# Performance work log

Measured on AMD Instinct MI355X. Metric: run time of the kernel, lower is better.

The kernel has to match this reference:

```python
import jax, jax.numpy as jnp
import numpy as np

B, L, T = 8, 1024, 10
K = 1.0                 # soft_sign sharpness (config.k)
S = float(np.log(9.0))  # self.s
W_PEN = 1.0             # self.w


def soft_sign(x):
    return jax.nn.sigmoid(2.0 * K * x)


def mlp2(f, W1, b1, W2, b2):
    # pointwise 2-layer MLP with ReLU after each layer; output dim 1 -> squeeze
    h = jax.nn.relu(jnp.einsum('...i,oi->...o', f, W1) + b1)
    return jax.nn.relu(jnp.einsum('...i,oi->...o', h, W2) + b2)[..., 0]


def setup_inputs() -> dict:
    key = jax.random.key(0)
    ks = jax.random.split(key, 16)
    u = jax.random.normal(ks[0], (B, L, L), jnp.float32)
    x = jax.random.uniform(ks[1], (B, L, 4), jnp.float32)
    p = lambda k, s: (jax.random.normal(k, s, jnp.float32) * 0.5)
    return dict(
        u=u, x=x, timesteps=T,
        aW1=p(ks[2], (T, 3, 3)), ab1=p(ks[3], (T, 3)), aW2=p(ks[4], (T, 1, 3)), ab2=p(ks[5], (T, 1)),
        rW1=p(ks[6], (T, 3, 3)), rb1=p(ks[7], (T, 3)), rW2=p(ks[8], (T, 1, 3)), rb2=p(ks[9], (T, 1)),
        lW1=p(ks[10], (T, 3, 2)), lb1=p(ks[11], (T, 3)), lW2=p(ks[12], (T, 1, 3)), lb2=p(ks[13], (T, 1)),
    )


def reference(u, x, timesteps, aW1, ab1, aW2, ab2, rW1, rb1, rW2, rb2, lW1, lb1, lW2, lb2):
    # constraint matrix m: sum of symmetrized outer products of base channels
    ba, bu, bc, bg = x[:, :, 0], x[:, :, 1], x[:, :, 2], x[:, :, 3]
    def sym_outer(p, q):
        o = jnp.einsum('bi,bj->bij', p, q)
        return o + o.swapaxes(-1, -2)
    m = sym_outer(ba, bu) + sym_outer(bc, bg) + sym_outer(bu, bg)

    def contact(ah):
        aa = ah * ah
        return (aa + aa.swapaxes(-1, -2)) * 0.5 * m

    uu = soft_sign(u - S) * u
    a_hat = jax.nn.sigmoid(uu) * soft_sign(uu - S)
    a = contact(a_hat)
    lmbd = W_PEN * jax.nn.relu(jnp.sum(a, -1) - 1.0)

    outs = []
    for t in range(timesteps):  # fixed unroll, distinct params per step
        grad_a = -uu * 0.5 + (lmbd * soft_sign(jnp.sum(a, -1) - 1.0))[..., None]
        grad = a_hat * m * (grad_a + grad_a.swapaxes(-1, -2))
        feats = jnp.stack([a_hat, grad, uu], -1)  # [B,L,L,3]
        ah_new = mlp2(feats, aW1[t], ab1[t], aW2[t], ab2[t])
        rho = mlp2(feats, rW1[t], rb1[t], rW2[t], rb2[t])
        ah_new = jnp.clip(jax.nn.relu(jnp.abs(ah_new) - rho), -1.0, 1.0)
        a = contact(ah_new)
        lg = jax.nn.relu(jnp.sum(a, -1) - 1.0)
        lmbd = mlp2(jnp.stack([lmbd, lg], -1), lW1[t], lb1[t], lW2[t], lb2[t])
        a_hat = ah_new
        outs.append(a)
    return jnp.stack(outs)  # [T,B,L,L] == a_t_list[1:]
```

## Files before the change

### kernel.cpp

```cpp
#include <hip/hip_runtime.h>
#include <hip/hip_bf16.h>

#define BB 8
#define LL 1024
#define TT 10
#define TILE 64
#define NTILE 16
#define NOFF 120
#define NBLK 1024
#define S_CONST 2.1972245773362196f

typedef __hip_bfloat16 bf16;

static __device__ __forceinline__ float sigm(float v) {
    return 1.0f / (1.0f + __expf(-v));
}
static __device__ __forceinline__ unsigned short f2bf(float v) {
    bf16 h = __float2bfloat16(v);
    unsigned short b; __builtin_memcpy(&b, &h, 2); return b;
}
static __device__ __forceinline__ float lo2f(unsigned int v) { return __uint_as_float(v << 16); }
static __device__ __forceinline__ float hi2f(unsigned int v) { return __uint_as_float(v & 0xffff0000u); }
static __device__ __forceinline__ unsigned int pk2(float uu, float ah) {
    return (unsigned int)f2bf(uu) | ((unsigned int)f2bf(ah) << 16);
}

#define RAWBAR() do { asm volatile("s_waitcnt lgkmcnt(0)" ::: "memory"); \
                      __builtin_amdgcn_s_barrier(); } while (0)

static __device__ __forceinline__ void wait_done(const unsigned int* dcnt) {
    for (int it = 0; it < (1 << 20); ++it) {
        if (__hip_atomic_load(dcnt, __ATOMIC_RELAXED, __HIP_MEMORY_SCOPE_AGENT) >= 16u)
            break;
        __builtin_amdgcn_s_sleep(4);
    }
}

static __device__ __forceinline__ float mlp3(float f0, float f1, float f2, const float* w) {
    float h0 = fmaxf(w[0]*f0 + w[1]*f1 + w[2]*f2 + w[9],  0.0f);
    float h1 = fmaxf(w[3]*f0 + w[4]*f1 + w[5]*f2 + w[10], 0.0f);
    float h2 = fmaxf(w[6]*f0 + w[7]*f1 + w[8]*f2 + w[11], 0.0f);
    return fmaxf(w[12]*h0 + w[13]*h1 + w[14]*h2 + w[15], 0.0f);
}
static __device__ __forceinline__ float ahnew_calc(float ah, float grad, float uuv, const float* w) {
    float va = mlp3(ah, grad, uuv, w);
    float vr = mlp3(ah, grad, uuv, w + 16);
    float v = fmaxf(fabsf(va) - vr, 0.0f);
    return fminf(v, 1.0f);
}

#define LOAD_W(tt) do { if (tid < 32) { int _t = (tt); float v; \
    if      (tid <  9) v = aW1[_t*9 + tid]; \
    else if (tid < 12) v = ab1[_t*3 + (tid-9)]; \
    else if (tid < 15) v = aW2[_t*3 + (tid-12)]; \
    else if (tid < 16) v = ab2[_t]; \
    else if (tid < 25) v = rW1[_t*9 + (tid-16)]; \
    else if (tid < 28) v = rb1[_t*3 + (tid-25)]; \
    else if (tid < 31) v = rW2[_t*3 + (tid-28)]; \
    else               v = rb2[_t]; \
    w[tid] = v; } } while (0)

#define LAMBDA_PHASE(ROWI, ROWJ) do { if (tid < 128) { \
    int row = (tid < 64) ? ((ROWI) + tid) : ((ROWJ) + tid - 64); \
    float rsv = __hip_atomic_load(&rs_cur[b*LL + row], __ATOMIC_RELAXED, __HIP_MEMORY_SCOPE_AGENT); \
    float lg = fmaxf(rsv - 1.0f, 0.0f); \
    if (t == 0) lam = lg; \
    else { int o = t - 1; \
        float h0 = fmaxf(lW1[o*6+0]*lam + lW1[o*6+1]*lg + lb1[o*3+0], 0.0f); \
        float h1 = fmaxf(lW1[o*6+2]*lam + lW1[o*6+3]*lg + lb1[o*3+1], 0.0f); \
        float h2 = fmaxf(lW1[o*6+4]*lam + lW1[o*6+5]*lg + lb1[o*3+2], 0.0f); \
        lam = fmaxf(lW2[o*3+0]*h0 + lW2[o*3+1]*h1 + lW2[o*3+2]*h2 + lb2[o], 0.0f); } \
    float lsv = lam * sigm(2.0f*(rsv - 1.0f)); \
    if (tid < 64) { lsI[tid] = lsv; rsIb[tid] = 0.0f; } \
    else          { lsJ[tid-64] = lsv; rsJb[tid-64] = 0.0f; } } } while (0)

__global__ __launch_bounds__(256, 4) void k_main(
        const float* __restrict__ u, const float* __restrict__ x,
        float* __restrict__ rs, unsigned int* __restrict__ done,
        float* __restrict__ out,
        const float* __restrict__ aW1, const float* __restrict__ ab1,
        const float* __restrict__ aW2, const float* __restrict__ ab2,
        const float* __restrict__ rW1, const float* __restrict__ rb1,
        const float* __restrict__ rW2, const float* __restrict__ rb2,
        const float* __restrict__ lW1, const float* __restrict__ lb1,
        const float* __restrict__ lW2, const float* __restrict__ lb2) {
    __shared__ unsigned int stA[TILE * 65];
    __shared__ unsigned int stB[TILE * 65];
    __shared__ float buf[16 * 65];
    __shared__ float xIl[4 * TILE];
    __shared__ float lsI[TILE], lsJ[TILE];
    __shared__ float rsIb[TILE], rsJb[TILE];
    __shared__ float w[32];

    int gid = blockIdx.x, tid = threadIdx.x;
    int c = tid & 63, rg = tid >> 6;
    float lam = 0.0f;

    if (gid < BB * NOFF) {
        int b = gid / NOFF, po = gid % NOFF;
        int i = 0; while (po >= NTILE - 1 - i) { po -= NTILE - 1 - i; i++; }
        int I = i, J = i + 1 + po;
        int Ib = I * TILE, Jb = J * TILE;

        float xc0 = x[((size_t)b*LL + Jb + c)*4 + 0], xc1 = x[((size_t)b*LL + Jb + c)*4 + 1];
        float xc2 = x[((size_t)b*LL + Jb + c)*4 + 2], xc3 = x[((size_t)b*LL + Jb + c)*4 + 3];
        float bu_c = xc1, bg_c = xc3, s1_c = xc0 + xc3, s2_c = xc2 + xc1;
        { int row = tid >> 2, k2 = tid & 3;
          xIl[k2*TILE + row] = x[((size_t)b*LL + Ib + row)*4 + k2]; }

        size_t ubIJ = ((size_t)b*LL + Ib)*LL + Jb;
        size_t ubJI = ((size_t)b*LL + Jb)*LL + Ib;
        #pragma unroll
        for (int k = 0; k < 16; k++) {
            int r = rg + 4*k;
            float uv  = u[ubIJ + (size_t)r*LL + c];
            float uuv = sigm(2.0f*(uv - S_CONST))*uv;
            float ah  = sigm(uuv)*sigm(2.0f*(uuv - S_CONST));
            stA[r*65 + c] = pk2(uuv, ah);
            uv  = u[ubJI + (size_t)r*LL + c];
            uuv = sigm(2.0f*(uv - S_CONST))*uv;
            ah  = sigm(uuv)*sigm(2.0f*(uuv - S_CONST));
            stB[r*65 + c] = pk2(uuv, ah);
        }
        if (tid < 64) rsIb[tid] = 0.0f; else if (tid < 128) rsJb[tid-64] = 0.0f;
        __syncthreads();

        {
            float aval[16]; float rsJacc = 0.0f;
            #pragma unroll
            for (int k = 0; k < 16; k++) {
                int r = rg + 4*k;
                float ah_ij = hi2f(stA[r*65 + c]);
                float ah_ji = hi2f(stB[c*65 + r]);
                float m = xIl[0*TILE+r]*bu_c + xIl[2*TILE+r]*bg_c
                        + xIl[1*TILE+r]*s1_c + xIl[3*TILE+r]*s2_c;
                float a0 = 0.5f*(ah_ij*ah_ij + ah_ji*ah_ji)*m;
                aval[k] = a0; rsJacc += a0;
            }
            atomicAdd(&rsJb[c], rsJacc);
            #pragma unroll
            for (int p = 0; p < 4; p++) {
                #pragma unroll
                for (int kk = 0; kk < 4; kk++) { int jj = rg + 4*kk; buf[jj*65 + c] = aval[4*p + kk]; }
                RAWBAR();
                { int jj = tid & 15, cc0 = tid >> 4;
                  float part = 0.0f;
                  #pragma unroll
                  for (int s = 0; s < 4; s++) part += buf[jj*65 + (cc0 + 16*s)];
                  atomicAdd(&rsIb[16*p + jj], part); }
                RAWBAR();
            }
            if (tid < 64) atomicAdd(&rs[b*LL + Ib + tid], rsIb[tid]);
            else if (tid < 128) atomicAdd(&rs[b*LL + Jb + (tid-64)], rsJb[tid-64]);
            if (tid < 128) {
                asm volatile("s_waitcnt vmcnt(0)" ::: "memory");
                if (tid == 0)
                    __hip_atomic_fetch_add(&done[(0*128 + b*16 + I)*16], 1u, __ATOMIC_RELAXED, __HIP_MEMORY_SCOPE_AGENT);
                if (tid == 64)
                    __hip_atomic_fetch_add(&done[(0*128 + b*16 + J)*16], 1u, __ATOMIC_RELAXED, __HIP_MEMORY_SCOPE_AGENT);
            }
        }

        for (int t = 0; t < TT; t++) {
            LOAD_W(t);
            if (tid == 0)  wait_done(&done[((size_t)t*128 + b*16 + I)*16]);
            if (tid == 64) wait_done(&done[((size_t)t*128 + b*16 + J)*16]);
            RAWBAR();
            asm volatile("" ::: "memory");
            const float* rs_cur = rs + (size_t)t*BB*LL;
            LAMBDA_PHASE(Ib, Jb);
            RAWBAR();

            size_t outBase = (((size_t)t*BB + b)*LL)*LL;
            bool last = (t == TT-1);
            float aval[16]; float rsJacc = 0.0f;
            #pragma unroll
            for (int k = 0; k < 16; k++) {
                int r = rg + 4*k;
                unsigned int vA = stA[r*65 + c], vB = stB[c*65 + r];
                float uu_ij = lo2f(vA), ah_ij = hi2f(vA);
                float uu_ji = lo2f(vB), ah_ji = hi2f(vB);
                float m = xIl[0*TILE+r]*bu_c + xIl[2*TILE+r]*bg_c
                        + xIl[1*TILE+r]*s1_c + xIl[3*TILE+r]*s2_c;
                float gsum = -0.5f*(uu_ij + uu_ji) + lsI[r] + lsJ[c];
                float an_ij = ahnew_calc(ah_ij, ah_ij*m*gsum, uu_ij, w);
                float an_ji = ahnew_calc(ah_ji, ah_ji*m*gsum, uu_ji, w);
                float a_val = 0.5f*(an_ij*an_ij + an_ji*an_ji)*m;
                ((unsigned short*)stA)[(r*65 + c)*2 + 1] = f2bf(an_ij);
                ((unsigned short*)stB)[(c*65 + r)*2 + 1] = f2bf(an_ji);
                __builtin_nontemporal_store(a_val, &out[outBase + (size_t)(Ib+r)*LL + (Jb+c)]);
                aval[k] = a_val; rsJacc += a_val;
            }
            atomicAdd(&rsJb[c], rsJacc);

            #pragma unroll
            for (int p = 0; p < 4; p++) {
                #pragma unroll
                for (int kk = 0; kk < 4; kk++) { int jj = rg + 4*kk; buf[jj*65 + c] = aval[4*p + kk]; }
                RAWBAR();
                { int jj = tid & 15, cc0 = tid >> 4;
                  float part = 0.0f;
                  #pragma unroll
                  for (int s = 0; s < 4; s++) {
                      int cc = cc0 + 16*s;
                      float v = buf[jj*65 + cc];
                      __builtin_nontemporal_store(v, &out[outBase + (size_t)(Jb+cc)*LL + (Ib + 16*p + jj)]);
                      part += v;
                  }
                  if (!last) atomicAdd(&rsIb[16*p + jj], part); }
                RAWBAR();
            }
            if (!last) {
                float* rs_next = rs + (size_t)(t+1)*BB*LL;
                if (tid < 128) {
                    if (tid < 64) atomicAdd(&rs_next[b*LL + Ib + tid], rsIb[tid]);
                    else          atomicAdd(&rs_next[b*LL + Jb + (tid-64)], rsJb[tid-64]);
                    asm volatile("s_waitcnt vmcnt(0)" ::: "memory");
                    if (tid == 0)
                        __hip_atomic_fetch_add(&done[((size_t)(t+1)*128 + b*16 + I)*16], 1u, __ATOMIC_RELAXED, __HIP_MEMORY_SCOPE_AGENT);
                    if (tid == 64)
                        __hip_atomic_fetch_add(&done[((size_t)(t+1)*128 + b*16 + J)*16], 1u, __ATOMIC_RELAXED, __HIP_MEMORY_SCOPE_AGENT);
                }
            }
        }
    } else {
        int d = gid - BB*NOFF;
        int g0 = 2*d;
        int b = g0 >> 4;
        int TA = g0 & 15, TB = (g0 & 15) + 1;
        int Ab = TA * TILE, Bb = TB * TILE;
        float* xIlB = buf;

        float t0, t1, t2, t3;
        t0 = x[((size_t)b*LL + Ab + c)*4 + 0]; t1 = x[((size_t)b*LL + Ab + c)*4 + 1];
        t2 = x[((size_t)b*LL + Ab + c)*4 + 2]; t3 = x[((size_t)b*LL + Ab + c)*4 + 3];
        float buA = t1, bgA = t3, s1A = t0 + t3, s2A = t2 + t1;
        t0 = x[((size_t)b*LL + Bb + c)*4 + 0]; t1 = x[((size_t)b*LL + Bb + c)*4 + 1];
        t2 = x[((size_t)b*LL + Bb + c)*4 + 2]; t3 = x[((size_t)b*LL + Bb + c)*4 + 3];
        float buB = t1, bgB = t3, s1B = t0 + t3, s2B = t2 + t1;
        { int row = tid >> 2, k2 = tid & 3;
          xIl [k2*TILE + row] = x[((size_t)b*LL + Ab + row)*4 + k2];
          xIlB[k2*TILE + row] = x[((size_t)b*LL + Bb + row)*4 + k2]; }

        size_t ubA = ((size_t)b*LL + Ab)*LL + Ab;
        size_t ubB = ((size_t)b*LL + Bb)*LL + Bb;
        #pragma unroll
        for (int k = 0; k < 16; k++) {
            int r = rg + 4*k;
            float uv  = u[ubA + (size_t)r*LL + c];
            float uuv = sigm(2.0f*(uv - S_CONST))*uv;
            float ah  = sigm(uuv)*sigm(2.0f*(uuv - S_CONST));
            stA[r*65 + c] = pk2(uuv, ah);
            uv  = u[ubB + (size_t)r*LL + c];
            uuv = sigm(2.0f*(uv - S_CONST))*uv;
            ah  = sigm(uuv)*sigm(2.0f*(uuv - S_CONST));
            stB[r*65 + c] = pk2(uuv, ah);
        }
        if (tid < 64) rsIb[tid] = 0.0f; else if (tid < 128) rsJb[tid-64] = 0.0f;
        __syncthreads();
        {
            float accA = 0.0f, accB = 0.0f;
            #pragma unroll
            for (int k = 0; k < 16; k++) {
                int r = rg + 4*k;
                float aij = hi2f(stA[r*65 + c]), aji = hi2f(stA[c*65 + r]);
                float m = xIl[0*TILE+r]*buA + xIl[2*TILE+r]*bgA
                        + xIl[1*TILE+r]*s1A + xIl[3*TILE+r]*s2A;
                accA += 0.5f*(aij*aij + aji*aji)*m;
                aij = hi2f(stB[r*65 + c]); aji = hi2f(stB[c*65 + r]);
                m = xIlB[0*TILE+r]*buB + xIlB[2*TILE+r]*bgB
                  + xIlB[1*TILE+r]*s1B + xIlB[3*TILE+r]*s2B;
                accB += 0.5f*(aij*aij + aji*aji)*m;
            }
            atomicAdd(&rsIb[c], accA);
            atomicAdd(&rsJb[c], accB);
            RAWBAR();
            if (tid < 64) atomicAdd(&rs[b*LL + Ab + tid], rsIb[tid]);
            else if (tid < 128) atomicAdd(&rs[b*LL + Bb + (tid-64)], rsJb[tid-64]);
            if (tid < 128) {
                asm volatile("s_waitcnt vmcnt(0)" ::: "memory");
                if (tid == 0)
                    __hip_atomic_fetch_add(&done[(0*128 + b*16 + TA)*16], 1u, __ATOMIC_RELAXED, __HIP_MEMORY_SCOPE_AGENT);
                if (tid == 64)
                    __hip_atomic_fetch_add(&done[(0*128 + b*16 + TB)*16], 1u, __ATOMIC_RELAXED, __HIP_MEMORY_SCOPE_AGENT);
            }
        }

        for (int t = 0; t < TT; t++) {
            LOAD_W(t);
            if (tid == 0)  wait_done(&done[((size_t)t*128 + b*16 + TA)*16]);
            if (tid == 64) wait_done(&done[((size_t)t*128 + b*16 + TB)*16]);
            RAWBAR();
            asm volatile("" ::: "memory");
            const float* rs_cur = rs + (size_t)t*BB*LL;
            LAMBDA_PHASE(Ab, Bb);
            RAWBAR();

            size_t outBase = (((size_t)t*BB + b)*LL)*LL;
            bool last = (t == TT-1);

            unsigned int vT[16];
            #pragma unroll
            for (int k = 0; k < 16; k++) vT[k] = stA[c*65 + (rg + 4*k)];
            RAWBAR();
            float acc = 0.0f;
            #pragma unroll
            for (int k = 0; k < 16; k++) {
                int r = rg + 4*k;
                unsigned int vO = stA[r*65 + c];
                float uu_ij = lo2f(vO), ah_ij = hi2f(vO);
                float uu_ji = lo2f(vT[k]), ah_ji = hi2f(vT[k]);
                float m = xIl[0*TILE+r]*buA + xIl[2*TILE+r]*bgA
                        + xIl[1*TILE+r]*s1A + xIl[3*TILE+r]*s2A;
                float gsum = -0.5f*(uu_ij + uu_ji) + lsI[r] + lsI[c];
                float an_ij = ahnew_calc(ah_ij, ah_ij*m*gsum, uu_ij, w);
                float an_ji = ahnew_calc(ah_ji, ah_ji*m*gsum, uu_ji, w);
                float a_val = 0.5f*(an_ij*an_ij + an_ji*an_ji)*m;
                ((unsigned short*)stA)[(r*65 + c)*2 + 1] = f2bf(an_ij);
                __builtin_nontemporal_store(a_val, &out[outBase + (size_t)(Ab+r)*LL + (Ab+c)]);
                acc += a_val;
            }
            if (!last) atomicAdd(&rsIb[c], acc);

            #pragma unroll
            for (int k = 0; k < 16; k++) vT[k] = stB[c*65 + (rg + 4*k)];
            RAWBAR();
            acc = 0.0f;
            #pragma unroll
            for (int k = 0; k < 16; k++) {
                int r = rg + 4*k;
                unsigned int vO = stB[r*65 + c];
                float uu_ij = lo2f(vO), ah_ij = hi2f(vO);
                float uu_ji = lo2f(vT[k]), ah_ji = hi2f(vT[k]);
                float m = xIlB[0*TILE+r]*buB + xIlB[2*TILE+r]*bgB
                        + xIlB[1*TILE+r]*s1B + xIlB[3*TILE+r]*s2B;
                float gsum = -0.5f*(uu_ij + uu_ji) + lsJ[r] + lsJ[c];
                float an_ij = ahnew_calc(ah_ij, ah_ij*m*gsum, uu_ij, w);
                float an_ji = ahnew_calc(ah_ji, ah_ji*m*gsum, uu_ji, w);
                float a_val = 0.5f*(an_ij*an_ij + an_ji*an_ji)*m;
                ((unsigned short*)stB)[(r*65 + c)*2 + 1] = f2bf(an_ij);
                __builtin_nontemporal_store(a_val, &out[outBase + (size_t)(Bb+r)*LL + (Bb+c)]);
                acc += a_val;
            }
            if (!last) {
                atomicAdd(&rsJb[c], acc);
                RAWBAR();
                float* rs_next = rs + (size_t)(t+1)*BB*LL;
                if (tid < 128) {
                    if (tid < 64) atomicAdd(&rs_next[b*LL + Ab + tid], rsIb[tid]);
                    else          atomicAdd(&rs_next[b*LL + Bb + (tid-64)], rsJb[tid-64]);
                    asm volatile("s_waitcnt vmcnt(0)" ::: "memory");
                    if (tid == 0)
                        __hip_atomic_fetch_add(&done[((size_t)(t+1)*128 + b*16 + TA)*16], 1u, __ATOMIC_RELAXED, __HIP_MEMORY_SCOPE_AGENT);
                    if (tid == 64)
                        __hip_atomic_fetch_add(&done[((size_t)(t+1)*128 + b*16 + TB)*16], 1u, __ATOMIC_RELAXED, __HIP_MEMORY_SCOPE_AGENT);
                }
            }
        }
    }
}

extern "C" void kernel_launch(void* const* d_in, const int* in_sizes, int n_in,
                              void* d_out, int out_size, void* d_ws, size_t ws_size,
                              hipStream_t stream) {
    const float* u   = (const float*)d_in[0];
    const float* x   = (const float*)d_in[1];
    const float* aW1 = (const float*)d_in[3];
    const float* ab1 = (const float*)d_in[4];
    const float* aW2 = (const float*)d_in[5];
    const float* ab2 = (const float*)d_in[6];
    const float* rW1 = (const float*)d_in[7];
    const float* rb1 = (const float*)d_in[8];
    const float* rW2 = (const float*)d_in[9];
    const float* rb2 = (const float*)d_in[10];
    const float* lW1 = (const float*)d_in[11];
    const float* lb1 = (const float*)d_in[12];
    const float* lW2 = (const float*)d_in[13];
    const float* lb2 = (const float*)d_in[14];
    float* out = (float*)d_out;

    float* rs = (float*)d_ws;
    unsigned int* done = (unsigned int*)(rs + (size_t)TT*BB*LL);
    size_t zbytes = (size_t)TT*BB*LL*sizeof(float) + (size_t)TT*128*16*sizeof(unsigned int);
    hipMemsetAsync(rs, 0, zbytes, stream);

    hipLaunchKernelGGL(k_main, dim3(NBLK), dim3(256), 0, stream,
                       u, x, rs, done, out,
                       aW1, ab1, aW2, ab2, rW1, rb1, rW2, rb2,
                       lW1, lb1, lW2, lb2);
}
```

Before: 551.3 us.

## Keep tile state in registers, one diagonal tile per block, shrink LDS

The per-tile packed (uu, a_hat) state moves out of shared memory into per-thread registers; both the tile and its transpose are held by each thread. Shared memory drops to a single staging buffer, which allows launch bounds of 5 blocks per CU. The row-sum reduction and transposed output store are collapsed from four barrier-separated passes into one. Diagonal work is split into one block per tile instead of pairs, adding 64 blocks. The cost is higher register pressure, which may cause spills under the tighter launch bound.

```diff
diff --git a/kernel.cpp b/kernel.cpp
--- a/kernel.cpp
+++ b/kernel.cpp
@@ -7,7 +7,8 @@
 #define TILE 64
 #define NTILE 16
 #define NOFF 120
-#define NBLK 1024
+#define NOFFT (BB*NOFF)
+#define NBLK (NOFFT + BB*NTILE)
 #define S_CONST 2.1972245773362196f
 
 typedef __hip_bfloat16 bf16;
@@ -34,6 +35,10 @@
             break;
         __builtin_amdgcn_s_sleep(4);
     }
+}
+static __device__ __forceinline__ void add_done(unsigned int* done, int t, int b, int tile) {
+    __hip_atomic_fetch_add(&done[((size_t)t*128 + b*16 + tile)*16], 1u,
+                           __ATOMIC_RELAXED, __HIP_MEMORY_SCOPE_AGENT);
 }
 
 static __device__ __forceinline__ float mlp3(float f0, float f1, float f2, const float* w) {
@@ -60,21 +65,17 @@
     else               v = rb2[_t]; \
     w[tid] = v; } } while (0)
 
-#define LAMBDA_PHASE(ROWI, ROWJ) do { if (tid < 128) { \
-    int row = (tid < 64) ? ((ROWI) + tid) : ((ROWJ) + tid - 64); \
-    float rsv = __hip_atomic_load(&rs_cur[b*LL + row], __ATOMIC_RELAXED, __HIP_MEMORY_SCOPE_AGENT); \
-    float lg = fmaxf(rsv - 1.0f, 0.0f); \
+#define LAM_UPDATE(rsv) do { \
+    float lg = fmaxf((rsv) - 1.0f, 0.0f); \
     if (t == 0) lam = lg; \
     else { int o = t - 1; \
         float h0 = fmaxf(lW1[o*6+0]*lam + lW1[o*6+1]*lg + lb1[o*3+0], 0.0f); \
         float h1 = fmaxf(lW1[o*6+2]*lam + lW1[o*6+3]*lg + lb1[o*3+1], 0.0f); \
         float h2 = fmaxf(lW1[o*6+4]*lam + lW1[o*6+5]*lg + lb1[o*3+2], 0.0f); \
         lam = fmaxf(lW2[o*3+0]*h0 + lW2[o*3+1]*h1 + lW2[o*3+2]*h2 + lb2[o], 0.0f); } \
-    float lsv = lam * sigm(2.0f*(rsv - 1.0f)); \
-    if (tid < 64) { lsI[tid] = lsv; rsIb[tid] = 0.0f; } \
-    else          { lsJ[tid-64] = lsv; rsJb[tid-64] = 0.0f; } } } while (0)
-
-__global__ __launch_bounds__(256, 4) void k_main(
+    } while (0)
+
+__global__ __launch_bounds__(256, 5) void k_main(
         const float* __restrict__ u, const float* __restrict__ x,
         float* __restrict__ rs, unsigned int* __restrict__ done,
         float* __restrict__ out,
@@ -84,30 +85,29 @@
         const float* __restrict__ rW2, const float* __restrict__ rb2,
         const float* __restrict__ lW1, const float* __restrict__ lb1,
         const float* __restrict__ lW2, const float* __restrict__ lb2) {
-    __shared__ unsigned int stA[TILE * 65];
-    __shared__ unsigned int stB[TILE * 65];
-    __shared__ float buf[16 * 65];
+    __shared__ unsigned int bufU[TILE * 65];
     __shared__ float xIl[4 * TILE];
     __shared__ float lsI[TILE], lsJ[TILE];
     __shared__ float rsIb[TILE], rsJb[TILE];
     __shared__ float w[32];
+    float* buff = (float*)bufU;
 
     int gid = blockIdx.x, tid = threadIdx.x;
     int c = tid & 63, rg = tid >> 6;
     float lam = 0.0f;
 
-    if (gid < BB * NOFF) {
+    if (gid < NOFFT) {
         int b = gid / NOFF, po = gid % NOFF;
         int i = 0; while (po >= NTILE - 1 - i) { po -= NTILE - 1 - i; i++; }
         int I = i, J = i + 1 + po;
         int Ib = I * TILE, Jb = J * TILE;
 
-        float xc0 = x[((size_t)b*LL + Jb + c)*4 + 0], xc1 = x[((size_t)b*LL + Jb + c)*4 + 1];
-        float xc2 = x[((size_t)b*LL + Jb + c)*4 + 2], xc3 = x[((size_t)b*LL + Jb + c)*4 + 3];
-        float bu_c = xc1, bg_c = xc3, s1_c = xc0 + xc3, s2_c = xc2 + xc1;
+        float4 xc4 = ((const float4*)x)[(size_t)b*LL + Jb + c];
+        float bu_c = xc4.y, bg_c = xc4.w, s1_c = xc4.x + xc4.w, s2_c = xc4.z + xc4.y;
         { int row = tid >> 2, k2 = tid & 3;
           xIl[k2*TILE + row] = x[((size_t)b*LL + Ib + row)*4 + k2]; }
 
+        unsigned int vIJ[16], vJI[16];
         size_t ubIJ = ((size_t)b*LL + Ib)*LL + Jb;
         size_t ubJI = ((size_t)b*LL + Jb)*LL + Ib;
         #pragma unroll
@@ -116,48 +116,44 @@
             float uv  = u[ubIJ + (size_t)r*LL + c];
             float uuv = sigm(2.0f*(uv - S_CONST))*uv;
             float ah  = sigm(uuv)*sigm(2.0f*(uuv - S_CONST));
-            stA[r*65 + c] = pk2(uuv, ah);
+            vIJ[k] = pk2(uuv, ah);
             uv  = u[ubJI + (size_t)r*LL + c];
             uuv = sigm(2.0f*(uv - S_CONST))*uv;
             ah  = sigm(uuv)*sigm(2.0f*(uuv - S_CONST));
-            stB[r*65 + c] = pk2(uuv, ah);
+            bufU[r*65 + c] = pk2(uuv, ah);
         }
         if (tid < 64) rsIb[tid] = 0.0f; else if (tid < 128) rsJb[tid-64] = 0.0f;
-        __syncthreads();
+        RAWBAR();
+        #pragma unroll
+        for (int k = 0; k < 16; k++) vJI[k] = bufU[c*65 + (rg + 4*k)];
+        RAWBAR();
 
         {
-            float aval[16]; float rsJacc = 0.0f;
+            float rsJacc = 0.0f;
             #pragma unroll
             for (int k = 0; k < 16; k++) {
                 int r = rg + 4*k;
-                float ah_ij = hi2f(stA[r*65 + c]);
-                float ah_ji = hi2f(stB[c*65 + r]);
+                float ah_ij = hi2f(vIJ[k]), ah_ji = hi2f(vJI[k]);
                 float m = xIl[0*TILE+r]*bu_c + xIl[2*TILE+r]*bg_c
                         + xIl[1*TILE+r]*s1_c + xIl[3*TILE+r]*s2_c;
                 float a0 = 0.5f*(ah_ij*ah_ij + ah_ji*ah_ji)*m;
-                aval[k] = a0; rsJacc += a0;
+                buff[r*65 + c] = a0;
+                rsJacc += a0;
             }
             atomicAdd(&rsJb[c], rsJacc);
-            #pragma unroll
-            for (int p = 0; p < 4; p++) {
-                #pragma unroll
-                for (int kk = 0; kk < 4; kk++) { int jj = rg + 4*kk; buf[jj*65 + c] = aval[4*p + kk]; }
-                RAWBAR();
-                { int jj = tid & 15, cc0 = tid >> 4;
-                  float part = 0.0f;
-                  #pragma unroll
-                  for (int s = 0; s < 4; s++) part += buf[jj*65 + (cc0 + 16*s)];
-                  atomicAdd(&rsIb[16*p + jj], part); }
-                RAWBAR();
-            }
+            RAWBAR();
+            { int jj = tid & 63, cc0 = tid >> 6;
+              float part = 0.0f;
+              #pragma unroll
+              for (int s = 0; s < 16; s++) part += buff[jj*65 + (cc0*16 + s)];
+              atomicAdd(&rsIb[jj], part); }
+            RAWBAR();
             if (tid < 64) atomicAdd(&rs[b*LL + Ib + tid], rsIb[tid]);
             else if (tid < 128) atomicAdd(&rs[b*LL + Jb + (tid-64)], rsJb[tid-64]);
             if (tid < 128) {
                 asm volatile("s_waitcnt vmcnt(0)" ::: "memory");
-                if (tid == 0)
-                    __hip_atomic_fetch_add(&done[(0*128 + b*16 + I)*16], 1u, __ATOMIC_RELAXED, __HIP_MEMORY_SCOPE_AGENT);
-                if (tid == 64)
-                    __hip_atomic_fetch_add(&done[(0*128 + b*16 + J)*16], 1u, __ATOMIC_RELAXED, __HIP_MEMORY_SCOPE_AGENT);
+                if (tid == 0)  add_done(done, 0, b, I);
+                if (tid == 64) add_done(done, 0, b, J);
             }
         }
 
@@ -166,18 +162,24 @@
             if (tid == 0)  wait_done(&done[((size_t)t*128 + b*16 + I)*16]);
             if (tid == 64) wait_done(&done[((size_t)t*128 + b*16 + J)*16]);
             RAWBAR();
-            asm volatile("" ::: "memory");
             const float* rs_cur = rs + (size_t)t*BB*LL;
-            LAMBDA_PHASE(Ib, Jb);
+            if (tid < 128) {
+                int row = (tid < 64) ? (Ib + tid) : (Jb + tid - 64);
+                float rsv = __hip_atomic_load(&rs_cur[b*LL + row], __ATOMIC_RELAXED, __HIP_MEMORY_SCOPE_AGENT);
+                LAM_UPDATE(rsv);
+                float lsv = lam * sigm(2.0f*(rsv - 1.0f));
+                if (tid < 64) { lsI[tid] = lsv; rsIb[tid] = 0.0f; }
+                else          { lsJ[tid-64] = lsv; rsJb[tid-64] = 0.0f; }
+            }
             RAWBAR();
 
             size_t outBase = (((size_t)t*BB + b)*LL)*LL;
             bool last = (t == TT-1);
-            float aval[16]; float rsJacc = 0.0f;
+            float rsJacc = 0.0f;
             #pragma unroll
             for (int k = 0; k < 16; k++) {
                 int r = rg + 4*k;
-                unsigned int vA = stA[r*65 + c], vB = stB[c*65 + r];
+                unsigned int vA = vIJ[k], vB = vJI[k];
                 float uu_ij = lo2f(vA), ah_ij = hi2f(vA);
                 float uu_ji = lo2f(vB), ah_ji = hi2f(vB);
                 float m = xIl[0*TILE+r]*bu_c + xIl[2*TILE+r]*bg_c
@@ -186,174 +188,125 @@
                 float an_ij = ahnew_calc(ah_ij, ah_ij*m*gsum, uu_ij, w);
                 float an_ji = ahnew_calc(ah_ji, ah_ji*m*gsum, uu_ji, w);
                 float a_val = 0.5f*(an_ij*an_ij + an_ji*an_ji)*m;
-                ((unsigned short*)stA)[(r*65 + c)*2 + 1] = f2bf(an_ij);
-                ((unsigned short*)stB)[(c*65 + r)*2 + 1] = f2bf(an_ji);
+                vIJ[k] = ((unsigned int)f2bf(an_ij) << 16) | (vA & 0xffffu);
+                vJI[k] = ((unsigned int)f2bf(an_ji) << 16) | (vB & 0xffffu);
                 __builtin_nontemporal_store(a_val, &out[outBase + (size_t)(Ib+r)*LL + (Jb+c)]);
-                aval[k] = a_val; rsJacc += a_val;
-            }
-            atomicAdd(&rsJb[c], rsJacc);
-
-            #pragma unroll
-            for (int p = 0; p < 4; p++) {
-                #pragma unroll
-                for (int kk = 0; kk < 4; kk++) { int jj = rg + 4*kk; buf[jj*65 + c] = aval[4*p + kk]; }
+                buff[r*65 + c] = a_val;
+                rsJacc += a_val;
+            }
+            if (!last) atomicAdd(&rsJb[c], rsJacc);
+            RAWBAR();
+            { int jj = tid & 63, cc0 = tid >> 6;
+              float part = 0.0f;
+              #pragma unroll
+              for (int s = 0; s < 16; s++) {
+                  int cc = cc0*16 + s;
+                  float v = buff[jj*65 + cc];
+                  __builtin_nontemporal_store(v, &out[outBase + (size_t)(Jb+cc)*LL + (Ib + jj)]);
+                  part += v;
+              }
+              if (!last) atomicAdd(&rsIb[jj], part); }
+            if (!last) {
                 RAWBAR();
-                { int jj = tid & 15, cc0 = tid >> 4;
-                  float part = 0.0f;
-                  #pragma unroll
-                  for (int s = 0; s < 4; s++) {
-                      int cc = cc0 + 16*s;
-                      float v = buf[jj*65 + cc];
-                      __builtin_nontemporal_store(v, &out[outBase + (size_t)(Jb+cc)*LL + (Ib + 16*p + jj)]);
-                      part += v;
-                  }
-                  if (!last) atomicAdd(&rsIb[16*p + jj], part); }
-                RAWBAR();
-            }
-            if (!last) {
                 float* rs_next = rs + (size_t)(t+1)*BB*LL;
                 if (tid < 128) {
                     if (tid < 64) atomicAdd(&rs_next[b*LL + Ib + tid], rsIb[tid]);
                     else          atomicAdd(&rs_next[b*LL + Jb + (tid-64)], rsJb[tid-64]);
                     asm volatile("s_waitcnt vmcnt(0)" ::: "memory");
-                    if (tid == 0)
-                        __hip_atomic_fetch_add(&done[((size_t)(t+1)*128 + b*16 + I)*16], 1u, __ATOMIC_RELAXED, __HIP_MEMORY_SCOPE_AGENT);
-                    if (tid == 64)
-                        __hip_atomic_fetch_add(&done[((size_t)(t+1)*128 + b*16 + J)*16], 1u, __ATOMIC_RELAXED, __HIP_MEMORY_SCOPE_AGENT);
+                    if (tid == 0)  add_done(done, t+1, b, I);
+                    if (tid == 64) add_done(done, t+1, b, J);
                 }
             }
         }
     } else {
-        int d = gid - BB*NOFF;
-        int g0 = 2*d;
-        int b = g0 >> 4;
-        int TA = g0 & 15, TB = (g0 & 15) + 1;
-        int Ab = TA * TILE, Bb = TB * TILE;
-        float* xIlB = buf;
-
-        float t0, t1, t2, t3;
-        t0 = x[((size_t)b*LL + Ab + c)*4 + 0]; t1 = x[((size_t)b*LL + Ab + c)*4 + 1];
-        t2 = x[((size_t)b*LL + Ab + c)*4 + 2]; t3 = x[((size_t)b*LL + Ab + c)*4 + 3];
-        float buA = t1, bgA = t3, s1A = t0 + t3, s2A = t2 + t1;
-        t0 = x[((size_t)b*LL + Bb + c)*4 + 0]; t1 = x[((size_t)b*LL + Bb + c)*4 + 1];
-        t2 = x[((size_t)b*LL + Bb + c)*4 + 2]; t3 = x[((size_t)b*LL + Bb + c)*4 + 3];
-        float buB = t1, bgB = t3, s1B = t0 + t3, s2B = t2 + t1;
+        int d = gid - NOFFT;
+        int b = d >> 4, tI = d & 15;
+        int Ab = tI * TILE;
+
+        float4 xc4 = ((const float4*)x)[(size_t)b*LL + Ab + c];
+        float ac = xc4.x, uc = xc4.y, cc_ = xc4.z, gc = xc4.w;
         { int row = tid >> 2, k2 = tid & 3;
-          xIl [k2*TILE + row] = x[((size_t)b*LL + Ab + row)*4 + k2];
-          xIlB[k2*TILE + row] = x[((size_t)b*LL + Bb + row)*4 + k2]; }
-
+          xIl[k2*TILE + row] = x[((size_t)b*LL + Ab + row)*4 + k2]; }
+
+        unsigned int vO[16], vT[16];
         size_t ubA = ((size_t)b*LL + Ab)*LL + Ab;
-        size_t ubB = ((size_t)b*LL + Bb)*LL + Bb;
         #pragma unroll
         for (int k = 0; k < 16; k++) {
             int r = rg + 4*k;
             float uv  = u[ubA + (size_t)r*LL + c];
             float uuv = sigm(2.0f*(uv - S_CONST))*uv;
             float ah  = sigm(uuv)*sigm(2.0f*(uuv - S_CONST));
-            stA[r*65 + c] = pk2(uuv, ah);
-            uv  = u[ubB + (size_t)r*LL + c];
-            uuv = sigm(2.0f*(uv - S_CONST))*uv;
-            ah  = sigm(uuv)*sigm(2.0f*(uuv - S_CONST));
-            stB[r*65 + c] = pk2(uuv, ah);
-        }
-        if (tid < 64) rsIb[tid] = 0.0f; else if (tid < 128) rsJb[tid-64] = 0.0f;
-        __syncthreads();
+            unsigned int p = pk2(uuv, ah);
+            vO[k] = p;
+            bufU[r*65 + c] = p;
+        }
+        if (tid < 64) rsIb[tid] = 0.0f;
+        RAWBAR();
+        #pragma unroll
+        for (int k = 0; k < 16; k++) vT[k] = bufU[c*65 + (rg + 4*k)];
+
         {
-            float accA = 0.0f, accB = 0.0f;
-            #pragma unroll
-            for (int k = 0; k < 16; k++) {
-                int r = rg + 4*k;
-                float aij = hi2f(stA[r*65 + c]), aji = hi2f(stA[c*65 + r]);
-                float m = xIl[0*TILE+r]*buA + xIl[2*TILE+r]*bgA
-                        + xIl[1*TILE+r]*s1A + xIl[3*TILE+r]*s2A;
-                accA += 0.5f*(aij*aij + aji*aji)*m;
-                aij = hi2f(stB[r*65 + c]); aji = hi2f(stB[c*65 + r]);
-                m = xIlB[0*TILE+r]*buB + xIlB[2*TILE+r]*bgB
-                  + xIlB[1*TILE+r]*s1B + xIlB[3*TILE+r]*s2B;
-                accB += 0.5f*(aij*aij + aji*aji)*m;
-            }
-            atomicAdd(&rsIb[c], accA);
-            atomicAdd(&rsJb[c], accB);
-            RAWBAR();
-            if (tid < 64) atomicAdd(&rs[b*LL + Ab + tid], rsIb[tid]);
-            else if (tid < 128) atomicAdd(&rs[b*LL + Bb + (tid-64)], rsJb[tid-64]);
-            if (tid < 128) {
-                asm volatile("s_waitcnt vmcnt(0)" ::: "memory");
-                if (tid == 0)
-                    __hip_atomic_fetch_add(&done[(0*128 + b*16 + TA)*16], 1u, __ATOMIC_RELAXED, __HIP_MEMORY_SCOPE_AGENT);
-                if (tid == 64)
-                    __hip_atomic_fetch_add(&done[(0*128 + b*16 + TB)*16], 1u, __ATOMIC_RELAXED, __HIP_MEMORY_SCOPE_AGENT);
-            }
-        }
-
-        for (int t = 0; t < TT; t++) {
-            LOAD_W(t);
-            if (tid == 0)  wait_done(&done[((size_t)t*128 + b*16 + TA)*16]);
-            if (tid == 64) wait_done(&done[((size_t)t*128 + b*16 + TB)*16]);
-            RAWBAR();
-            asm volatile("" ::: "memory");
-            const float* rs_cur = rs + (size_t)t*BB*LL;
-            LAMBDA_PHASE(Ab, Bb);
-            RAWBAR();
-
-            size_t outBase = (((size_t)t*BB + b)*LL)*LL;
-            bool last = (t == TT-1);
-
-            unsigned int vT[16];
-            #pragma unroll
-            for (int k = 0; k < 16; k++) vT[k] = stA[c*65 + (rg + 4*k)];
-            RAWBAR();
             float acc = 0.0f;
             #pragma unroll
             for (int k = 0; k < 16; k++) {
                 int r = rg + 4*k;
-                unsigned int vO = stA[r*65 + c];
-                float uu_ij = lo2f(vO), ah_ij = hi2f(vO);
-                float uu_ji = lo2f(vT[k]), ah_ji = hi2f(vT[k]);
-                float m = xIl[0*TILE+r]*buA + xIl[2*TILE+r]*bgA
-                        + xIl[1*TILE+r]*s1A + xIl[3*TILE+r]*s2A;
-                float gsum = -0.5f*(uu_ij + uu_ji) + lsI[r] + lsI[c];
+                float ah_ij = hi2f(vO[k]), ah_ji = hi2f(vT[k]);
+                float ar = xIl[0*TILE+r], ur = xIl[1*TILE+r];
+                float cr = xIl[2*TILE+r], gr = xIl[3*TILE+r];
+                float m = (ar*uc + ac*ur) + (cr*gc + cc_*gr) + (ur*gc + uc*gr);
+                acc += 0.5f*(ah_ij*ah_ij + ah_ji*ah_ji)*m;
+            }
+            atomicAdd(&rsIb[c], acc);
+            RAWBAR();
+            if (tid < 64) {
+                atomicAdd(&rs[b*LL + Ab + tid], rsIb[tid]);
+                asm volatile("s_waitcnt vmcnt(0)" ::: "memory");
+                if (tid == 0) add_done(done, 0, b, tI);
+            }
+        }
+
+        for (int t = 0; t < TT; t++) {
+            LOAD_W(t);
+            if (tid == 0) wait_done(&done[((size_t)t*128 + b*16 + tI)*16]);
+            RAWBAR();
+            const float* rs_cur = rs + (size_t)t*BB*LL;
+            if (tid < 64) {
+                float rsv = __hip_atomic_load(&rs_cur[b*LL + Ab + tid], __ATOMIC_RELAXED, __HIP_MEMORY_SCOPE_AGENT);
+                LAM_UPDATE(rsv);
+                lsI[tid] = lam * sigm(2.0f*(rsv - 1.0f));
+                rsIb[tid] = 0.0f;
+            }
+            RAWBAR();
+
+            size_t outBase = (((size_t)t*BB + b)*LL)*LL;
+            bool last = (t == TT-1);
+            float acc = 0.0f;
+            #pragma unroll
+            for (int k = 0; k < 16; k++) {
+                int r = rg + 4*k;
+                unsigned int vA = vO[k], vB = vT[k];
+                float uu_ij = lo2f(vA), ah_ij = hi2f(vA);
+                float uu_ji = lo2f(vB), ah_ji = hi2f(vB);
+                float ar = xIl[0*TILE+r], ur = xIl[1*TILE+r];
+                float cr = xIl[2*TILE+r], gr = xIl[3*TILE+r];
+                float m = (ar*uc + ac*ur) + (cr*gc + cc_*gr) + (ur*gc + uc*gr);
+                float lsum = lsI[r] + lsI[c];
+                float gsum = -0.5f*(uu_ij + uu_ji) + lsum;
                 float an_ij = ahnew_calc(ah_ij, ah_ij*m*gsum, uu_ij, w);
                 float an_ji = ahnew_calc(ah_ji, ah_ji*m*gsum, uu_ji, w);
                 float a_val = 0.5f*(an_ij*an_ij + an_ji*an_ji)*m;
-                ((unsigned short*)stA)[(r*65 + c)*2 + 1] = f2bf(an_ij);
+                vO[k] = ((unsigned int)f2bf(an_ij) << 16) | (vA & 0xffffu);
+                vT[k] = ((unsigned int)f2bf(an_ji) << 16) | (vB & 0xffffu);
                 __builtin_nontemporal_store(a_val, &out[outBase + (size_t)(Ab+r)*LL + (Ab+c)]);
                 acc += a_val;
             }
-            if (!last) atomicAdd(&rsIb[c], acc);
-
-            #pragma unroll
-            for (int k = 0; k < 16; k++) vT[k] = stB[c*65 + (rg + 4*k)];
-            RAWBAR();
-            acc = 0.0f;
-            #pragma unroll
-            for (int k = 0; k < 16; k++) {
-                int r = rg + 4*k;
-                unsigned int vO = stB[r*65 + c];
-                float uu_ij = lo2f(vO), ah_ij = hi2f(vO);
-                float uu_ji = lo2f(vT[k]), ah_ji = hi2f(vT[k]);
-                float m = xIlB[0*TILE+r]*buB + xIlB[2*TILE+r]*bgB
-                        + xIlB[1*TILE+r]*s1B + xIlB[3*TILE+r]*s2B;
-                float gsum = -0.5f*(uu_ij + uu_ji) + lsJ[r] + lsJ[c];
-                float an_ij = ahnew_calc(ah_ij, ah_ij*m*gsum, uu_ij, w);
-                float an_ji = ahnew_calc(ah_ji, ah_ji*m*gsum, uu_ji, w);
-                float a_val = 0.5f*(an_ij*an_ij + an_ji*an_ji)*m;
-                ((unsigned short*)stB)[(r*65 + c)*2 + 1] = f2bf(an_ij);
-                __builtin_nontemporal_store(a_val, &out[outBase + (size_t)(Bb+r)*LL + (Bb+c)]);
-                acc += a_val;
-            }
             if (!last) {
-                atomicAdd(&rsJb[c], acc);
+                atomicAdd(&rsIb[c], acc);
                 RAWBAR();
-                float* rs_next = rs + (size_t)(t+1)*BB*LL;
-                if (tid < 128) {
-                    if (tid < 64) atomicAdd(&rs_next[b*LL + Ab + tid], rsIb[tid]);
-                    else          atomicAdd(&rs_next[b*LL + Bb + (tid-64)], rsJb[tid-64]);
+                if (tid < 64) {
+                    atomicAdd(&rs[(size_t)(t+1)*BB*LL + b*LL + Ab + tid], rsIb[tid]);
                     asm volatile("s_waitcnt vmcnt(0)" ::: "memory");
-                    if (tid == 0)
-                        __hip_atomic_fetch_add(&done[((size_t)(t+1)*128 + b*16 + TA)*16], 1u, __ATOMIC_RELAXED, __HIP_MEMORY_SCOPE_AGENT);
-                    if (tid == 64)
-                        __hip_atomic_fetch_add(&done[((size_t)(t+1)*128 + b*16 + TB)*16], 1u, __ATOMIC_RELAXED, __HIP_MEMORY_SCOPE_AGENT);
+                    if (tid == 0) add_done(done, t+1, b, tI);
                 }
             }
         }
```

After: 698.1 us. 1.27x slower.
